# Kernel optimization log

Measured on AMD Instinct MI355X. Metric: run time of the kernel, lower is better.

## Reference

```python
import jax, jax.numpy as jnp
import numpy as np


def _maxpool2(x):
    # x: [B, C, H, W] -> 2x2 max pool, stride 2
    b, c, h, w = x.shape
    return x.reshape(b, c, h // 2, 2, w // 2, 2).max(axis=(3, 5))


def _conv1x1(x, w, b):
    # x: [B, Cin, H, W], w: [Cout, Cin], b: [Cout]
    return jnp.einsum('bchw,oc->bohw', x, w) + b[None, :, None, None]


def setup_inputs() -> dict:
    key = jax.random.key(0)
    ks = jax.random.split(key, 8)
    C = 64
    B, H, W = 2, 128, 128
    s = 1.0 / np.sqrt(C)
    return {
        'x': jax.random.normal(ks[0], (B, C, H, W), jnp.float32),
        'w_theta': jax.random.normal(ks[1], (C // 8, C), jnp.float32) * s,
        'b_theta': jax.random.normal(ks[2], (C // 8,), jnp.float32) * s,
        'w_phi': jax.random.normal(ks[3], (C // 8, C), jnp.float32) * s,
        'b_phi': jax.random.normal(ks[4], (C // 8,), jnp.float32) * s,
        'w_g': jax.random.normal(ks[5], (C, C), jnp.float32) * s,
        'b_g': jax.random.normal(ks[6], (C,), jnp.float32) * s,
        'sigma_ratio': jnp.zeros((1,), jnp.float32) + 0.5,
    }


def reference(x, w_theta, b_theta, w_phi, b_phi, w_g, b_g, sigma_ratio):
    b, c, h, w = x.shape
    n = h * w
    # queries: [B, N, C//8]
    theta = _conv1x1(x, w_theta, b_theta).reshape(b, c // 8, n).transpose(0, 2, 1)
    # pooled keys: [B, C//8, N//4]
    phi = _maxpool2(_conv1x1(x, w_phi, b_phi)).reshape(b, c // 8, n // 4)
    # attention: [B, N, N//4] (unscaled, as in original)
    attn = jax.nn.softmax(jnp.einsum('bnd,bdm->bnm', theta, phi), axis=-1)
    # pooled values: [B, N//4, C]
    g = _maxpool2(_conv1x1(x, w_g, b_g)).reshape(b, c, n // 4).transpose(0, 2, 1)
    attn_g = jnp.einsum('bnm,bmc->bnc', attn, g)  # [B, N, C]
    attn_g = attn_g.transpose(0, 2, 1).reshape(b, c, h, w)
    return x + sigma_ratio * attn_g
```

## Files before the change

### kernel.cpp

```cpp
#include <hip/hip_runtime.h>
#include <hip/hip_bf16.h>

typedef _Float16 half8 __attribute__((ext_vector_type(8)));
typedef _Float16 f16x8 __attribute__((ext_vector_type(8)));
typedef __bf16 bf16x8 __attribute__((ext_vector_type(8)));
typedef float f32x16 __attribute__((ext_vector_type(16)));
typedef unsigned uint2v __attribute__((ext_vector_type(2)));
typedef short short2v __attribute__((ext_vector_type(2)));

#define NPIX 16384
#define NPOOL 4096
#define BN 32768
#define KSPLIT 4
#define CHUNK 1024
#define NSTEP 8
#define LOG2E 1.44269504088896340736f

__device__ inline f32x16 mfma16(half8 a, half8 b, f32x16 c) {
  return __builtin_amdgcn_mfma_f32_32x32x16_f16(a, b, c, 0, 0, 0);
}
__device__ inline f32x16 mfma16b(bf16x8 a, bf16x8 b, f32x16 c) {
  return __builtin_amdgcn_mfma_f32_32x32x16_bf16(a, b, c, 0, 0, 0);
}
__device__ inline float fast_exp2(float x) {
#if __has_builtin(__builtin_amdgcn_exp2f)
  return __builtin_amdgcn_exp2f(x);
#else
  return exp2f(x);
#endif
}
__device__ inline unsigned cvt_pk_bf16(float lo, float hi) {
  unsigned r;
  asm("v_cvt_pk_bf16_f32 %0, %1, %2" : "=v"(r) : "v"(lo), "v"(hi));
  return r;
}
__device__ inline float lsum_acc(unsigned u, float acc) {
#if __has_builtin(__builtin_amdgcn_fdot2_f32_bf16)
  const short2v ones = {(short)0x3F80, (short)0x3F80};
  return __builtin_amdgcn_fdot2_f32_bf16(__builtin_bit_cast(short2v, u), ones,
                                         acc, false);
#else
  unsigned lo = u << 16, hi = u & 0xFFFF0000u;
  return acc + __builtin_bit_cast(float, lo) + __builtin_bit_cast(float, hi);
#endif
}

__global__ __launch_bounds__(256) void prep_kernel(
    const float* __restrict__ x,
    const float* __restrict__ w_theta, const float* __restrict__ b_theta,
    const float* __restrict__ w_phi, const float* __restrict__ b_phi,
    const float* __restrict__ w_g, const float* __restrict__ b_g,
    _Float16* __restrict__ qf, _Float16* __restrict__ phiT,
    __bf16* __restrict__ gT) {
  __shared__ float xs[64][256];
  int bid = blockIdx.x;
  int oh = bid & 1;
  int pr = (bid >> 1) & 63;
  int b  = bid >> 7;
  int t = threadIdx.x;

  const float* xb = x + (size_t)b * 64 * NPIX + pr * 256;
#pragma unroll 8
  for (int c = 0; c < 64; c++) xs[c][t] = xb[(size_t)c * NPIX + t];
  __syncthreads();

  if (oh == 0) {
    float acc[8];
#pragma unroll
    for (int j = 0; j < 8; j++) acc[j] = b_theta[j];
#pragma unroll 4
    for (int c = 0; c < 64; c++) {
      float xv = xs[c][t];
#pragma unroll
      for (int j = 0; j < 8; j++) acc[j] += xv * w_theta[j * 64 + c];
    }
    half8 h;
#pragma unroll
    for (int j = 0; j < 8; j++) h[j] = (_Float16)(acc[j] * LOG2E);
    *(half8*)(qf + ((size_t)b * NPIX + pr * 256 + t) * 8) = h;
  }

  int pos = t & 63;
  int ocg = t >> 6;
  int oc0 = oh * 36 + ocg * 9;
  const float* wrow[9];
  float a0[9], a1[9], a2[9], a3[9];
#pragma unroll
  for (int j = 0; j < 9; j++) {
    int oc = oc0 + j;
    float bv;
    if (oc < 64) { wrow[j] = w_g + oc * 64; bv = b_g[oc]; }
    else         { wrow[j] = w_phi + (oc - 64) * 64; bv = b_phi[oc - 64]; }
    a0[j] = bv; a1[j] = bv; a2[j] = bv; a3[j] = bv;
  }
#pragma unroll 4
  for (int c = 0; c < 64; c++) {
    float2 lo = *(const float2*)&xs[c][2 * pos];
    float2 hi = *(const float2*)&xs[c][128 + 2 * pos];
#pragma unroll
    for (int j = 0; j < 9; j++) {
      float wv = wrow[j][c];
      a0[j] += wv * lo.x;
      a1[j] += wv * lo.y;
      a2[j] += wv * hi.x;
      a3[j] += wv * hi.y;
    }
  }
  int m = pr * 64 + pos;
#pragma unroll
  for (int j = 0; j < 9; j++) {
    int oc = oc0 + j;
    float v = fmaxf(fmaxf(a0[j], a1[j]), fmaxf(a2[j], a3[j]));
    if (oc < 64) gT[((size_t)b * 64 + oc) * NPOOL + m] = (__bf16)v;
    else         phiT[((size_t)b * NPOOL + m) * 8 + (oc - 64)] = (_Float16)v;
  }
}

__global__ __launch_bounds__(256, 4) void attn_kernel(
    const _Float16* __restrict__ qf, const _Float16* __restrict__ phiT,
    const __bf16* __restrict__ gT,
    float* __restrict__ part_l, _Float16* __restrict__ part_o) {
  __shared__ __bf16 lds_g[2][128 * 64];
  int bx = blockIdx.x;
  int kc = bx & (KSPLIT - 1);
  int qt = (bx >> 2) & 127;
  int b  = bx >> 9;
  int tid = threadIdx.x;
  int lane = tid & 63;
  int w = tid >> 6;
  int q = lane & 31, hi = lane >> 5;
  int qg0 = qt * 128 + w * 32;
  size_t qrow = (size_t)b * NPIX + qg0 + q;

  half8 qfrag = {0, 0, 0, 0, 0, 0, 0, 0};
  if (!hi) qfrag = *(const half8*)(qf + qrow * 8);

  f32x16 oacc0, oacc1, zero16;
#pragma unroll
  for (int i = 0; i < 16; i++) { oacc0[i] = 0.f; oacc1[i] = 0.f; zero16[i] = 0.f; }
  float lsum = 0.f;

  int kb0 = kc * CHUNK;

  const __bf16* gbase0;
  const __bf16* gbase1;
  {
    int c0 = (w * 2 + 0) * 8 + (lane >> 3);
    int c1 = (w * 2 + 1) * 8 + (lane >> 3);
    int s  = (lane & 7) ^ (lane >> 3);
    gbase0 = gT + ((size_t)b * 64 + c0) * NPOOL + 8 * s;
    gbase1 = gT + ((size_t)b * 64 + c1) * NPOOL + 8 * s;
  }
#define STAGE(buf, kb)                                                        \
  do {                                                                        \
    __builtin_amdgcn_global_load_lds(                                         \
        (const __attribute__((address_space(1))) void*)(gbase0 + (kb)),       \
        (__attribute__((address_space(3))) void*)((char*)&lds_g[buf][0] +     \
                                                  (w * 2 + 0) * 1024),        \
        16, 0, 0);                                                            \
    __builtin_amdgcn_global_load_lds(                                         \
        (const __attribute__((address_space(1))) void*)(gbase1 + (kb)),       \
        (__attribute__((address_space(3))) void*)((char*)&lds_g[buf][0] +     \
                                                  (w * 2 + 1) * 1024),        \
        16, 0, 0);                                                            \
    __builtin_amdgcn_global_load_lds(                                         \
        (const __attribute__((address_space(1))) void*)(gbase0 + (kb) + 64),  \
        (__attribute__((address_space(3))) void*)((char*)&lds_g[buf][0] +     \
                                                  8192 + (w * 2 + 0) * 1024), \
        16, 0, 0);                                                            \
    __builtin_amdgcn_global_load_lds(                                         \
        (const __attribute__((address_space(1))) void*)(gbase1 + (kb) + 64),  \
        (__attribute__((address_space(3))) void*)((char*)&lds_g[buf][0] +     \
                                                  8192 + (w * 2 + 1) * 1024), \
        16, 0, 0);                                                            \
  } while (0)

  STAGE(0, kb0);
  __syncthreads();
  int cur = 0;

#pragma unroll 1
  for (int step = 0; step < NSTEP; ++step) {
    int kb = kb0 + step * 128;
    if (step + 1 < NSTEP) STAGE(cur ^ 1, kb + 128);
#pragma unroll
    for (int kk = 0; kk < 2; ++kk) {
      int kbb = kb + kk * 64;
      half8 aphi0 = {0, 0, 0, 0, 0, 0, 0, 0}, aphi1 = aphi0;
      if (!hi) {
        aphi0 = *(const half8*)(phiT + ((size_t)b * NPOOL + kbb + q) * 8);
        aphi1 = *(const half8*)(phiT + ((size_t)b * NPOOL + kbb + 32 + q) * 8);
      }
      const __bf16* ldsb = &lds_g[cur][kk * 4096];
#pragma unroll
      for (int sub = 0; sub < 2; ++sub) {
        half8 aphi = sub ? aphi1 : aphi0;
        f32x16 sacc = mfma16(aphi, qfrag, zero16);
        float p[16];
#pragma unroll
        for (int i = 0; i < 16; i++) p[i] = fast_exp2(sacc[i]);
#pragma unroll
        for (int halfk = 0; halfk < 2; ++halfk) {
          int pb = halfk * 8;
          unsigned A0 = cvt_pk_bf16(p[pb + 0], p[pb + 1]);
          unsigned A1 = cvt_pk_bf16(p[pb + 2], p[pb + 3]);
          unsigned B0 = cvt_pk_bf16(p[pb + 4], p[pb + 5]);
          unsigned B1 = cvt_pk_bf16(p[pb + 6], p[pb + 7]);
          lsum = lsum_acc(A0, lsum);
          lsum = lsum_acc(A1, lsum);
          lsum = lsum_acc(B0, lsum);
          lsum = lsum_acc(B1, lsum);
          union { unsigned u[4]; bf16x8 h; } pf;
#if __has_builtin(__builtin_amdgcn_permlane32_swap)
          uint2v r0 = __builtin_amdgcn_permlane32_swap(A0, B0, false, false);
          uint2v r1 = __builtin_amdgcn_permlane32_swap(A1, B1, false, false);
          pf.u[0] = r0[0]; pf.u[1] = r1[0]; pf.u[2] = r0[1]; pf.u[3] = r1[1];
#else
          unsigned xA0 = __shfl_xor(A0, 32), xA1 = __shfl_xor(A1, 32);
          unsigned xB0 = __shfl_xor(B0, 32), xB1 = __shfl_xor(B1, 32);
          pf.u[0] = hi ? xB0 : A0;
          pf.u[1] = hi ? xB1 : A1;
          pf.u[2] = hi ? B0 : xA0;
          pf.u[3] = hi ? B1 : xA1;
#endif
          int sread = sub * 4 + halfk * 2 + hi;
          __builtin_amdgcn_s_setprio(1);
#pragma unroll
          for (int ct = 0; ct < 2; ++ct) {
            int row = ct * 32 + q;
            bf16x8 ag = *(const bf16x8*)(ldsb + row * 64 +
                                         (((16 * sread) ^ ((row & 7) << 4)) >> 1));
            if (ct == 0) oacc0 = mfma16b(ag, pf.h, oacc0);
            else         oacc1 = mfma16b(ag, pf.h, oacc1);
          }
          __builtin_amdgcn_s_setprio(0);
        }
      }
    }
    if (step + 1 < NSTEP) { __syncthreads(); cur ^= 1; }
  }
  lsum += __shfl_xor(lsum, 32);
  float rl = 1.0f / lsum;
  if (!hi) part_l[(size_t)kc * BN + qrow] = lsum;
  _Float16* po = part_o + (((size_t)(kc * 2 + b) * NPIX) + qg0 + q) * 64;
#pragma unroll
  for (int ct = 0; ct < 2; ++ct) {
#pragma unroll
    for (int g = 0; g < 4; ++g) {
      float v0 = (ct ? oacc1[4 * g + 0] : oacc0[4 * g + 0]) * rl;
      float v1 = (ct ? oacc1[4 * g + 1] : oacc0[4 * g + 1]) * rl;
      float v2 = (ct ? oacc1[4 * g + 2] : oacc0[4 * g + 2]) * rl;
      float v3 = (ct ? oacc1[4 * g + 3] : oacc0[4 * g + 3]) * rl;
      uint2v u;
      u[0] = __builtin_bit_cast(unsigned, __builtin_amdgcn_cvt_pkrtz(v0, v1));
      u[1] = __builtin_bit_cast(unsigned, __builtin_amdgcn_cvt_pkrtz(v2, v3));
      *(uint2v*)(po + 32 * ct + 8 * g + 4 * hi) = u;
    }
  }
}

__global__ __launch_bounds__(256) void reduce_kernel(
    const float* __restrict__ part_l, const _Float16* __restrict__ part_o,
    const float* __restrict__ x, const float* __restrict__ sig,
    float* __restrict__ out) {
  int t = threadIdx.x;
  int cg = t >> 6;
  int qi = blockIdx.x * 64 + (t & 63);
  int b = qi >> 14, n = qi & (NPIX - 1);
  float lv[KSPLIT], L = 0.f;
#pragma unroll
  for (int kc = 0; kc < KSPLIT; kc++) {
    lv[kc] = part_l[(size_t)kc * BN + qi];
    L += lv[kc];
  }
  float o16[16];
#pragma unroll
  for (int j = 0; j < 16; j++) o16[j] = 0.f;
#pragma unroll
  for (int kc = 0; kc < KSPLIT; kc++) {
    const _Float16* po = part_o + (((size_t)(kc * 2 + b) * NPIX) + n) * 64 + cg * 16;
    f16x8 v0 = *(const f16x8*)po;
    f16x8 v1 = *(const f16x8*)(po + 8);
    float wv = lv[kc];
#pragma unroll
    for (int j = 0; j < 8; j++) {
      o16[j]     += wv * (float)v0[j];
      o16[8 + j] += wv * (float)v1[j];
    }
  }
  float scale = sig[0] / L;
#pragma unroll
  for (int j = 0; j < 16; j++) {
    int c = cg * 16 + j;
    size_t idx = ((size_t)b * 64 + c) * NPIX + n;
    out[idx] = x[idx] + scale * o16[j];
  }
}

extern "C" void kernel_launch(void* const* d_in, const int* in_sizes, int n_in,
                              void* d_out, int out_size, void* d_ws, size_t ws_size,
                              hipStream_t stream) {
  const float* x       = (const float*)d_in[0];
  const float* w_theta = (const float*)d_in[1];
  const float* b_theta = (const float*)d_in[2];
  const float* w_phi   = (const float*)d_in[3];
  const float* b_phi   = (const float*)d_in[4];
  const float* w_g     = (const float*)d_in[5];
  const float* b_g     = (const float*)d_in[6];
  const float* sigma   = (const float*)d_in[7];
  float* out = (float*)d_out;

  char* ws = (char*)d_ws;
  _Float16* qf     = (_Float16*)ws;
  _Float16* phiT   = (_Float16*)(ws + 524288);
  __bf16*   gT     = (__bf16*)(ws + 655360);
  float*    part_l = (float*)(ws + 1703936);
  _Float16* part_o = (_Float16*)(ws + 2228224);

  prep_kernel<<<256, 256, 0, stream>>>(x, w_theta, b_theta, w_phi, b_phi,
                                       w_g, b_g, qf, phiT, gT);
  attn_kernel<<<2 * 128 * KSPLIT, 256, 0, stream>>>(qf, phiT, gT,
                                                    part_l, part_o);
  reduce_kernel<<<512, 256, 0, stream>>>(part_l, part_o, x, sigma, out);
}
```

Before: 61.66 us.

## Split key chunk across warp pairs within block and combine partials via LDS

Each block now covers 64 queries instead of 128. Its four warps form two query groups of 32, and within each group the two warps split the block's key chunk in half. The two partial accumulators and row sums are merged through LDS at the end, and the grid doubles to 2048 blocks. This trades the shared g tile reuse across four query warps for more blocks and shorter per-warp serial loops. The cost is more global g traffic, the LDS combine step, and only two warps issuing the staging loads.

```diff
diff --git a/kernel.cpp b/kernel.cpp
--- a/kernel.cpp
+++ b/kernel.cpp
@@ -13,7 +13,7 @@
 #define BN 32768
 #define KSPLIT 4
 #define CHUNK 1024
-#define NSTEP 8
+#define NSTEPW 8
 #define LOG2E 1.44269504088896340736f
 
 __device__ inline f32x16 mfma16(half8 a, half8 b, f32x16 c) {
@@ -120,16 +120,17 @@
     const _Float16* __restrict__ qf, const _Float16* __restrict__ phiT,
     const __bf16* __restrict__ gT,
     float* __restrict__ part_l, _Float16* __restrict__ part_o) {
-  __shared__ __bf16 lds_g[2][128 * 64];
+  __shared__ __bf16 lds_g[2][2][4096];
   int bx = blockIdx.x;
   int kc = bx & (KSPLIT - 1);
-  int qt = (bx >> 2) & 127;
-  int b  = bx >> 9;
+  int qt = (bx >> 2) & 255;
+  int b  = bx >> 10;
   int tid = threadIdx.x;
   int lane = tid & 63;
   int w = tid >> 6;
+  int qh = w >> 1, qw = w & 1;
   int q = lane & 31, hi = lane >> 5;
-  int qg0 = qt * 128 + w * 32;
+  int qg0 = qt * 64 + qh * 32;
   size_t qrow = (size_t)b * NPIX + qg0 + q;
 
   half8 qfrag = {0, 0, 0, 0, 0, 0, 0, 0};
@@ -140,106 +141,102 @@
   for (int i = 0; i < 16; i++) { oacc0[i] = 0.f; oacc1[i] = 0.f; zero16[i] = 0.f; }
   float lsum = 0.f;
 
-  int kb0 = kc * CHUNK;
-
-  const __bf16* gbase0;
-  const __bf16* gbase1;
-  {
-    int c0 = (w * 2 + 0) * 8 + (lane >> 3);
-    int c1 = (w * 2 + 1) * 8 + (lane >> 3);
-    int s  = (lane & 7) ^ (lane >> 3);
-    gbase0 = gT + ((size_t)b * 64 + c0) * NPOOL + 8 * s;
-    gbase1 = gT + ((size_t)b * 64 + c1) * NPOOL + 8 * s;
-  }
-#define STAGE(buf, kb)                                                        \
+  int kb0 = kc * CHUNK + qw * (CHUNK / 2);
+
+  const __bf16* gsrc = gT + ((size_t)b * 64 + (lane >> 3)) * NPOOL +
+                       8 * ((lane & 7) ^ (lane >> 3));
+#define STAGE8(tile, buf, kb)                                                 \
   do {                                                                        \
-    __builtin_amdgcn_global_load_lds(                                         \
-        (const __attribute__((address_space(1))) void*)(gbase0 + (kb)),       \
-        (__attribute__((address_space(3))) void*)((char*)&lds_g[buf][0] +     \
-                                                  (w * 2 + 0) * 1024),        \
-        16, 0, 0);                                                            \
-    __builtin_amdgcn_global_load_lds(                                         \
-        (const __attribute__((address_space(1))) void*)(gbase1 + (kb)),       \
-        (__attribute__((address_space(3))) void*)((char*)&lds_g[buf][0] +     \
-                                                  (w * 2 + 1) * 1024),        \
-        16, 0, 0);                                                            \
-    __builtin_amdgcn_global_load_lds(                                         \
-        (const __attribute__((address_space(1))) void*)(gbase0 + (kb) + 64),  \
-        (__attribute__((address_space(3))) void*)((char*)&lds_g[buf][0] +     \
-                                                  8192 + (w * 2 + 0) * 1024), \
-        16, 0, 0);                                                            \
-    __builtin_amdgcn_global_load_lds(                                         \
-        (const __attribute__((address_space(1))) void*)(gbase1 + (kb) + 64),  \
-        (__attribute__((address_space(3))) void*)((char*)&lds_g[buf][0] +     \
-                                                  8192 + (w * 2 + 1) * 1024), \
-        16, 0, 0);                                                            \
+    _Pragma("unroll")                                                         \
+    for (int i_ = 0; i_ < 8; ++i_) {                                          \
+      __builtin_amdgcn_global_load_lds(                                       \
+          (const __attribute__((address_space(1))) void*)(                    \
+              gsrc + (size_t)i_ * 8 * NPOOL + (kb)),                          \
+          (__attribute__((address_space(3))) void*)(                          \
+              (char*)&lds_g[tile][buf][0] + i_ * 1024),                       \
+          16, 0, 0);                                                          \
+    }                                                                         \
   } while (0)
 
-  STAGE(0, kb0);
+  if (w < 2) STAGE8(w, 0, kb0);
   __syncthreads();
   int cur = 0;
 
 #pragma unroll 1
-  for (int step = 0; step < NSTEP; ++step) {
-    int kb = kb0 + step * 128;
-    if (step + 1 < NSTEP) STAGE(cur ^ 1, kb + 128);
-#pragma unroll
-    for (int kk = 0; kk < 2; ++kk) {
-      int kbb = kb + kk * 64;
-      half8 aphi0 = {0, 0, 0, 0, 0, 0, 0, 0}, aphi1 = aphi0;
-      if (!hi) {
-        aphi0 = *(const half8*)(phiT + ((size_t)b * NPOOL + kbb + q) * 8);
-        aphi1 = *(const half8*)(phiT + ((size_t)b * NPOOL + kbb + 32 + q) * 8);
+  for (int step = 0; step < NSTEPW; ++step) {
+    int kbb = kb0 + step * 64;
+    if (step + 1 < NSTEPW && w < 2) STAGE8(w, cur ^ 1, kbb + 64);
+    half8 aphi0 = {0, 0, 0, 0, 0, 0, 0, 0}, aphi1 = aphi0;
+    if (!hi) {
+      aphi0 = *(const half8*)(phiT + ((size_t)b * NPOOL + kbb + q) * 8);
+      aphi1 = *(const half8*)(phiT + ((size_t)b * NPOOL + kbb + 32 + q) * 8);
+    }
+    const __bf16* ldsb = &lds_g[qw][cur][0];
+#pragma unroll
+    for (int sub = 0; sub < 2; ++sub) {
+      half8 aphi = sub ? aphi1 : aphi0;
+      f32x16 sacc = mfma16(aphi, qfrag, zero16);
+      float p[16];
+#pragma unroll
+      for (int i = 0; i < 16; i++) p[i] = fast_exp2(sacc[i]);
+#pragma unroll
+      for (int halfk = 0; halfk < 2; ++halfk) {
+        int pb = halfk * 8;
+        unsigned A0 = cvt_pk_bf16(p[pb + 0], p[pb + 1]);
+        unsigned A1 = cvt_pk_bf16(p[pb + 2], p[pb + 3]);
+        unsigned B0 = cvt_pk_bf16(p[pb + 4], p[pb + 5]);
+        unsigned B1 = cvt_pk_bf16(p[pb + 6], p[pb + 7]);
+        lsum = lsum_acc(A0, lsum);
+        lsum = lsum_acc(A1, lsum);
+        lsum = lsum_acc(B0, lsum);
+        lsum = lsum_acc(B1, lsum);
+        union { unsigned u[4]; bf16x8 h; } pf;
+#if __has_builtin(__builtin_amdgcn_permlane32_swap)
+        uint2v r0 = __builtin_amdgcn_permlane32_swap(A0, B0, false, false);
+        uint2v r1 = __builtin_amdgcn_permlane32_swap(A1, B1, false, false);
+        pf.u[0] = r0[0]; pf.u[1] = r1[0]; pf.u[2] = r0[1]; pf.u[3] = r1[1];
+#else
+        unsigned xA0 = __shfl_xor(A0, 32), xA1 = __shfl_xor(A1, 32);
+        unsigned xB0 = __shfl_xor(B0, 32), xB1 = __shfl_xor(B1, 32);
+        pf.u[0] = hi ? xB0 : A0;
+        pf.u[1] = hi ? xB1 : A1;
+        pf.u[2] = hi ? B0 : xA0;
+        pf.u[3] = hi ? B1 : xA1;
+#endif
+        int sread = sub * 4 + halfk * 2 + hi;
+        __builtin_amdgcn_s_setprio(1);
+#pragma unroll
+        for (int ct = 0; ct < 2; ++ct) {
+          int row = ct * 32 + q;
+          bf16x8 ag = *(const bf16x8*)(ldsb + row * 64 +
+                                       (((16 * sread) ^ ((row & 7) << 4)) >> 1));
+          if (ct == 0) oacc0 = mfma16b(ag, pf.h, oacc0);
+          else         oacc1 = mfma16b(ag, pf.h, oacc1);
+        }
+        __builtin_amdgcn_s_setprio(0);
       }
-      const __bf16* ldsb = &lds_g[cur][kk * 4096];
-#pragma unroll
-      for (int sub = 0; sub < 2; ++sub) {
-        half8 aphi = sub ? aphi1 : aphi0;
-        f32x16 sacc = mfma16(aphi, qfrag, zero16);
-        float p[16];
-#pragma unroll
-        for (int i = 0; i < 16; i++) p[i] = fast_exp2(sacc[i]);
-#pragma unroll
-        for (int halfk = 0; halfk < 2; ++halfk) {
-          int pb = halfk * 8;
-          unsigned A0 = cvt_pk_bf16(p[pb + 0], p[pb + 1]);
-          unsigned A1 = cvt_pk_bf16(p[pb + 2], p[pb + 3]);
-          unsigned B0 = cvt_pk_bf16(p[pb + 4], p[pb + 5]);
-          unsigned B1 = cvt_pk_bf16(p[pb + 6], p[pb + 7]);
-          lsum = lsum_acc(A0, lsum);
-          lsum = lsum_acc(A1, lsum);
-          lsum = lsum_acc(B0, lsum);
-          lsum = lsum_acc(B1, lsum);
-          union { unsigned u[4]; bf16x8 h; } pf;
-#if __has_builtin(__builtin_amdgcn_permlane32_swap)
-          uint2v r0 = __builtin_amdgcn_permlane32_swap(A0, B0, false, false);
-          uint2v r1 = __builtin_amdgcn_permlane32_swap(A1, B1, false, false);
-          pf.u[0] = r0[0]; pf.u[1] = r1[0]; pf.u[2] = r0[1]; pf.u[3] = r1[1];
-#else
-          unsigned xA0 = __shfl_xor(A0, 32), xA1 = __shfl_xor(A1, 32);
-          unsigned xB0 = __shfl_xor(B0, 32), xB1 = __shfl_xor(B1, 32);
-          pf.u[0] = hi ? xB0 : A0;
-          pf.u[1] = hi ? xB1 : A1;
-          pf.u[2] = hi ? B0 : xA0;
-          pf.u[3] = hi ? B1 : xA1;
-#endif
-          int sread = sub * 4 + halfk * 2 + hi;
-          __builtin_amdgcn_s_setprio(1);
-#pragma unroll
-          for (int ct = 0; ct < 2; ++ct) {
-            int row = ct * 32 + q;
-            bf16x8 ag = *(const bf16x8*)(ldsb + row * 64 +
-                                         (((16 * sread) ^ ((row & 7) << 4)) >> 1));
-            if (ct == 0) oacc0 = mfma16b(ag, pf.h, oacc0);
-            else         oacc1 = mfma16b(ag, pf.h, oacc1);
-          }
-          __builtin_amdgcn_s_setprio(0);
-        }
-      }
-    }
-    if (step + 1 < NSTEP) { __syncthreads(); cur ^= 1; }
+    }
+    if (step + 1 < NSTEPW) { __syncthreads(); cur ^= 1; }
   }
   lsum += __shfl_xor(lsum, 32);
+
+  __syncthreads();
+  float* cl = (float*)&lds_g[0][0][0];
+  float* co = cl + 64;
+  if (qw == 1) {
+    if (!hi) cl[qh * 32 + q] = lsum;
+    float* my = co + (qh * 64 + lane) * 33;
+#pragma unroll
+    for (int i = 0; i < 16; i++) { my[i] = oacc0[i]; my[16 + i] = oacc1[i]; }
+  }
+  __syncthreads();
+  if (qw == 1) return;
+  lsum += cl[qh * 32 + q];
+  {
+    const float* pr = co + (qh * 64 + lane) * 33;
+#pragma unroll
+    for (int i = 0; i < 16; i++) { oacc0[i] += pr[i]; oacc1[i] += pr[16 + i]; }
+  }
   float rl = 1.0f / lsum;
   if (!hi) part_l[(size_t)kc * BN + qrow] = lsum;
   _Float16* po = part_o + (((size_t)(kc * 2 + b) * NPIX) + qg0 + q) * 64;
@@ -319,7 +316,7 @@
 
   prep_kernel<<<256, 256, 0, stream>>>(x, w_theta, b_theta, w_phi, b_phi,
                                        w_g, b_g, qf, phiT, gT);
-  attn_kernel<<<2 * 128 * KSPLIT, 256, 0, stream>>>(qf, phiT, gT,
+  attn_kernel<<<2 * 256 * KSPLIT, 256, 0, stream>>>(qf, phiT, gT,
                                                     part_l, part_o);
   reduce_kernel<<<512, 256, 0, stream>>>(part_l, part_o, x, sigma, out);
 }
```

Measured after the change: 64.35 us. +4.4%, slower.
